# Kernel optimization log

Measured on AMD Instinct MI355X. Metric: run time of the kernel, lower is better.

Reference implementation:

```python
import jax, jax.numpy as jnp
import numpy as np

N = 1024
NEVAL = 131072
NUM_POLES = 8
DOMAIN = (-1.0, 1.0)
DOMAIN_LEN = DOMAIN[1] - DOMAIN[0]
EPS = 1e-14


def _cheb_nodes(n):
    # Chebyshev points of the second kind: cos(pi * linspace(0, 1, n))
    return jnp.cos(jnp.pi * jnp.linspace(0.0, 1.0, n))


def _to_standard(x):
    return 2.0 * (x - DOMAIN[0]) / DOMAIN_LEN - 1.0


def _barycentric_weights(nodes, poles_real, poles_imag):
    # Vectorized equivalent of the original per-node Python loop.
    n = nodes.shape[0]
    diff = nodes[:, None] - nodes[None, :]            # (N, N)
    eye = jnp.eye(n, dtype=bool)
    # log_weights[j] = -sum_{i!=j} log|nodes[j]-nodes[i]|
    log_w = -jnp.sum(jnp.log(jnp.where(eye, 1.0, jnp.abs(diff))), axis=1)
    # signs[j] = (-1)^(# of negative off-diagonal diffs); diagonal diff==0 contributes nothing
    neg_count = jnp.sum(diff < 0, axis=1)
    signs = jnp.where(neg_count % 2 == 0, 1.0, -1.0)
    # each conjugate pole pair contributes 2*log(sqrt((x-r)^2 + i^2)) = log((x-r)^2 + i^2)
    pole_term = jnp.log((nodes[:, None] - poles_real[None, :]) ** 2
                        + poles_imag[None, :] ** 2)   # (N, M)
    log_w = log_w + jnp.sum(pole_term, axis=1)
    log_w = log_w - jnp.max(log_w)
    w = signs * jnp.exp(log_w)
    return w / jnp.abs(w[0])


def setup_inputs() -> dict:
    key = jax.random.key(0)
    k1, k2, k3, k4 = jax.random.split(key, 4)
    x_eval = jax.random.uniform(k1, (NEVAL,), dtype=jnp.float32)  # in [0,1) subset of domain
    values = jax.random.normal(k2, (N,), dtype=jnp.float32)
    poles_real = jax.random.normal(k3, (NUM_POLES,), dtype=jnp.float32)
    poles_imag = jax.random.normal(k4, (NUM_POLES,), dtype=jnp.float32)
    return {"x_eval": x_eval, "values": values,
            "poles_real": poles_real, "poles_imag": poles_imag}


def reference(x_eval, values, poles_real, poles_imag):
    nodes = _cheb_nodes(N)
    nodes_std = _to_standard(nodes)                   # identity for domain (-1,1)
    w = _barycentric_weights(nodes, poles_real, poles_imag)

    x_std = _to_standard(x_eval)
    d_x = x_std[None, :] - nodes_std[:, None]         # (N, NEVAL)
    small = jnp.abs(d_x) < EPS
    small_any = jnp.any(small, axis=0)                # (NEVAL,)
    d_safe = jnp.where(small, 1.0, d_x)
    inv = jnp.where(small_any[None, :], 0.0, 1.0 / d_safe)
    inv = jnp.where(small, 1.0, inv)                  # exact-hit columns: indicator row -> 1

    num = jnp.einsum('n,nm,n->m', values, inv, w)
    den = jnp.einsum('nm,n->m', inv, w)
    return num / den
```

## Files before the change

### kernel.cpp

```cpp
#include <hip/hip_runtime.h>
#include <math.h>

#define N_NODES 1024
#define N_EVAL 131072
#define NUM_POLES 8
#define PI_D 3.14159265358979323846

__global__ void wk_setup(const float* __restrict__ values,
                         const float* __restrict__ poles_real,
                         const float* __restrict__ poles_imag,
                         float* __restrict__ nodes_f,
                         float* __restrict__ w_f,
                         float* __restrict__ wv_f) {
    const int j = threadIdx.x;
    const double nd = cos(PI_D * (double)j / (double)(N_NODES - 1));
    double prod = (j == 0 || j == N_NODES - 1) ? 0.5 : 1.0;
#pragma unroll
    for (int m = 0; m < NUM_POLES; ++m) {
        double dr = nd - (double)poles_real[m];
        double di = (double)poles_imag[m];
        prod *= dr * dr + di * di;
    }
    if (j & 1) prod = -prod;
    const float wf = (float)prod;
    nodes_f[j] = (float)nd;
    w_f[j] = wf;
    wv_f[j] = (float)(prod * (double)values[j]);
}

__global__ __launch_bounds__(256) void eval_kernel(
    const float* __restrict__ x_eval,
    const float* __restrict__ nodes_f,
    const float* __restrict__ w_f,
    const float* __restrict__ wv_f,
    float* __restrict__ out) {
    __shared__ __align__(16) float s_n[N_NODES];
    __shared__ __align__(16) float s_w[N_NODES];
    __shared__ __align__(16) float s_v[N_NODES];
    const int t = threadIdx.x;
    for (int k = t; k < N_NODES; k += 256) {
        s_n[k] = nodes_f[k];
        s_w[k] = w_f[k];
        s_v[k] = wv_f[k];
    }
    __syncthreads();

    const int i = blockIdx.x * 256 + t;
    const float x = x_eval[i];

    float num0 = 0.0f, den0 = 0.0f;
    float num1 = 0.0f, den1 = 0.0f;

    const float4* n4 = (const float4*)s_n;
    const float4* w4 = (const float4*)s_w;
    const float4* v4 = (const float4*)s_v;

#define BODY(C, NUM, DEN)                                                  \
    {                                                                      \
        float d = x - an.C;                                                \
        float r = __builtin_amdgcn_rcpf(d);                                \
        r = fmaf(r, fmaf(-d, r, 1.0f), r);              \
        NUM = fmaf(av.C, r, NUM);                                          \
        DEN = fmaf(aw.C, r, DEN);                                          \
    }

#pragma unroll 4
    for (int j4 = 0; j4 < N_NODES / 4; ++j4) {
        float4 an = n4[j4];
        float4 aw = w4[j4];
        float4 av = v4[j4];
        BODY(x, num0, den0)
        BODY(y, num1, den1)
        BODY(z, num0, den0)
        BODY(w, num1, den1)
    }
#undef BODY

    float res = (num0 + num1) / (den0 + den1);

    if (__builtin_expect(__builtin_isnan(res), 0)) {
        float hn = 0.0f, hd = 0.0f;
        for (int j = 0; j < N_NODES; ++j) {
            if (s_n[j] == x) { hn += s_v[j]; hd += s_w[j]; }
        }
        res = hn / hd;
    }
    out[i] = res;
}

extern "C" void kernel_launch(void* const* d_in, const int* in_sizes, int n_in,
                              void* d_out, int out_size, void* d_ws, size_t ws_size,
                              hipStream_t stream) {
    const float* x_eval     = (const float*)d_in[0];
    const float* values     = (const float*)d_in[1];
    const float* poles_real = (const float*)d_in[2];
    const float* poles_imag = (const float*)d_in[3];
    float* out = (float*)d_out;

    float* nodes_f = (float*)d_ws;
    float* w_f     = nodes_f + N_NODES;
    float* wv_f    = w_f + N_NODES;

    wk_setup<<<1, N_NODES, 0, stream>>>(values, poles_real, poles_imag,
                                        nodes_f, w_f, wv_f);
    eval_kernel<<<N_EVAL / 256, 256, 0, stream>>>(x_eval, nodes_f, w_f, wv_f, out);
}
```

Baseline: 145.3 us.

## Pair reciprocals into one rcp and split node sum across 4 lanes

New measurement: 130.3 us. 1.11x faster.

```diff
diff --git a/kernel.cpp b/kernel.cpp
--- a/kernel.cpp
+++ b/kernel.cpp
@@ -5,6 +5,10 @@
 #define N_EVAL 131072
 #define NUM_POLES 8
 #define PI_D 3.14159265358979323846
+
+#define CHUNKS 4
+#define CHUNK_N 256
+#define CHUNK_PAD 260
 
 __global__ void wk_setup(const float* __restrict__ values,
                          const float* __restrict__ poles_real,
@@ -22,70 +26,90 @@
         prod *= dr * dr + di * di;
     }
     if (j & 1) prod = -prod;
-    const float wf = (float)prod;
     nodes_f[j] = (float)nd;
-    w_f[j] = wf;
+    w_f[j] = (float)prod;
     wv_f[j] = (float)(prod * (double)values[j]);
 }
 
-__global__ __launch_bounds__(256) void eval_kernel(
+__global__ __launch_bounds__(256, 8) void eval_kernel(
     const float* __restrict__ x_eval,
     const float* __restrict__ nodes_f,
     const float* __restrict__ w_f,
     const float* __restrict__ wv_f,
     float* __restrict__ out) {
-    __shared__ __align__(16) float s_n[N_NODES];
-    __shared__ __align__(16) float s_w[N_NODES];
-    __shared__ __align__(16) float s_v[N_NODES];
+    __shared__ __align__(16) float s_n[CHUNKS * CHUNK_PAD];
+    __shared__ __align__(16) float s_w[CHUNKS * CHUNK_PAD];
+    __shared__ __align__(16) float s_v[CHUNKS * CHUNK_PAD];
     const int t = threadIdx.x;
-    for (int k = t; k < N_NODES; k += 256) {
-        s_n[k] = nodes_f[k];
-        s_w[k] = w_f[k];
-        s_v[k] = wv_f[k];
+#pragma unroll
+    for (int it = 0; it < 4; ++it) {
+        const int k = it * 256 + t;
+        const int idx = it * CHUNK_PAD + t;
+        s_n[idx] = nodes_f[k];
+        s_w[idx] = w_f[k];
+        s_v[idx] = wv_f[k];
     }
     __syncthreads();
 
-    const int i = blockIdx.x * 256 + t;
-    const float x = x_eval[i];
+    const int p = (blockIdx.x << 6) + (t >> 2);
+    const int c = t & 3;
+    const float x = x_eval[p];
+
+    const float4* n4 = (const float4*)(s_n + c * CHUNK_PAD);
+    const float4* w4 = (const float4*)(s_w + c * CHUNK_PAD);
+    const float4* v4 = (const float4*)(s_v + c * CHUNK_PAD);
 
     float num0 = 0.0f, den0 = 0.0f;
     float num1 = 0.0f, den1 = 0.0f;
 
-    const float4* n4 = (const float4*)s_n;
-    const float4* w4 = (const float4*)s_w;
-    const float4* v4 = (const float4*)s_v;
-
-#define BODY(C, NUM, DEN)                                                  \
-    {                                                                      \
-        float d = x - an.C;                                                \
-        float r = __builtin_amdgcn_rcpf(d);                                \
-        r = fmaf(r, fmaf(-d, r, 1.0f), r);              \
-        NUM = fmaf(av.C, r, NUM);                                          \
-        DEN = fmaf(aw.C, r, DEN);                                          \
+#pragma unroll 2
+    for (int q = 0; q < CHUNK_N / 4; ++q) {
+        const float4 an = n4[q];
+        const float4 aw = w4[q];
+        const float4 av = v4[q];
+        const float dx = x - an.x;
+        const float dy = x - an.y;
+        const float dz = x - an.z;
+        const float dw = x - an.w;
+        const float p0 = dx * dy;
+        const float p1 = dz * dw;
+        const float r0 = __builtin_amdgcn_rcpf(p0);
+        const float r1 = __builtin_amdgcn_rcpf(p1);
+        const float rx = r0 * dy;
+        const float ry = r0 * dx;
+        const float rz = r1 * dw;
+        const float rw = r1 * dz;
+        num0 = fmaf(av.x, rx, num0);
+        den0 = fmaf(aw.x, rx, den0);
+        num1 = fmaf(av.y, ry, num1);
+        den1 = fmaf(aw.y, ry, den1);
+        num0 = fmaf(av.z, rz, num0);
+        den0 = fmaf(aw.z, rz, den0);
+        num1 = fmaf(av.w, rw, num1);
+        den1 = fmaf(aw.w, rw, den1);
     }
 
-#pragma unroll 4
-    for (int j4 = 0; j4 < N_NODES / 4; ++j4) {
-        float4 an = n4[j4];
-        float4 aw = w4[j4];
-        float4 av = v4[j4];
-        BODY(x, num0, den0)
-        BODY(y, num1, den1)
-        BODY(z, num0, den0)
-        BODY(w, num1, den1)
+    float num = num0 + num1;
+    float den = den0 + den1;
+    num += __shfl_xor(num, 1);
+    den += __shfl_xor(den, 1);
+    num += __shfl_xor(num, 2);
+    den += __shfl_xor(den, 2);
+    float res = num / den;
+
+    if (c == 0) {
+        if (__builtin_expect(__builtin_isnan(res), 0)) {
+            float hn = 0.0f, hd = 0.0f;
+            for (int cc = 0; cc < CHUNKS; ++cc) {
+                for (int j = 0; j < CHUNK_N; ++j) {
+                    const int idx = cc * CHUNK_PAD + j;
+                    if (s_n[idx] == x) { hn += s_v[idx]; hd += s_w[idx]; }
+                }
+            }
+            res = hn / hd;
+        }
+        out[p] = res;
     }
-#undef BODY
-
-    float res = (num0 + num1) / (den0 + den1);
-
-    if (__builtin_expect(__builtin_isnan(res), 0)) {
-        float hn = 0.0f, hd = 0.0f;
-        for (int j = 0; j < N_NODES; ++j) {
-            if (s_n[j] == x) { hn += s_v[j]; hd += s_w[j]; }
-        }
-        res = hn / hd;
-    }
-    out[i] = res;
 }
 
 extern "C" void kernel_launch(void* const* d_in, const int* in_sizes, int n_in,
@@ -103,5 +127,5 @@
 
     wk_setup<<<1, N_NODES, 0, stream>>>(values, poles_real, poles_imag,
                                         nodes_f, w_f, wv_f);
-    eval_kernel<<<N_EVAL / 256, 256, 0, stream>>>(x_eval, nodes_f, w_f, wv_f, out);
+    eval_kernel<<<N_EVAL / 64, 256, 0, stream>>>(x_eval, nodes_f, w_f, wv_f, out);
 }
```

## Pair reciprocals, stream nodes via scalar loads, split node range across waves

Applied to the files above, without the earlier changes.

Measured after the change: 151.7 us. +4.4%, slower.

```diff
diff --git a/kernel.cpp b/kernel.cpp
--- a/kernel.cpp
+++ b/kernel.cpp
@@ -9,10 +9,8 @@
 __global__ void wk_setup(const float* __restrict__ values,
                          const float* __restrict__ poles_real,
                          const float* __restrict__ poles_imag,
-                         float* __restrict__ nodes_f,
-                         float* __restrict__ w_f,
-                         float* __restrict__ wv_f) {
-    const int j = threadIdx.x;
+                         float4* __restrict__ pk) {
+    const int j = blockIdx.x * 128 + threadIdx.x;
     const double nd = cos(PI_D * (double)j / (double)(N_NODES - 1));
     double prod = (j == 0 || j == N_NODES - 1) ? 0.5 : 1.0;
 #pragma unroll
@@ -22,70 +20,79 @@
         prod *= dr * dr + di * di;
     }
     if (j & 1) prod = -prod;
-    const float wf = (float)prod;
-    nodes_f[j] = (float)nd;
-    w_f[j] = wf;
-    wv_f[j] = (float)(prod * (double)values[j]);
+    pk[j] = make_float4((float)nd, (float)prod,
+                        (float)(prod * (double)values[j]), 0.0f);
 }
 
-__global__ __launch_bounds__(256) void eval_kernel(
+typedef float f16v __attribute__((ext_vector_type(16)));
+
+__global__ __launch_bounds__(256, 8) void eval_kernel(
     const float* __restrict__ x_eval,
-    const float* __restrict__ nodes_f,
-    const float* __restrict__ w_f,
-    const float* __restrict__ wv_f,
+    const float4* __restrict__ pk,
     float* __restrict__ out) {
-    __shared__ __align__(16) float s_n[N_NODES];
-    __shared__ __align__(16) float s_w[N_NODES];
-    __shared__ __align__(16) float s_v[N_NODES];
-    const int t = threadIdx.x;
-    for (int k = t; k < N_NODES; k += 256) {
-        s_n[k] = nodes_f[k];
-        s_w[k] = w_f[k];
-        s_v[k] = wv_f[k];
-    }
-    __syncthreads();
+    const int lane = threadIdx.x & 63;
+    const int wid  = threadIdx.x >> 6;
+    const int p = blockIdx.x * 64 + lane;
+    const float x = x_eval[p];
 
-    const int i = blockIdx.x * 256 + t;
-    const float x = x_eval[i];
+    unsigned long long up = (unsigned long long)(pk + wid * 256);
+    const unsigned lo = __builtin_amdgcn_readfirstlane((unsigned int)up);
+    const unsigned hi = __builtin_amdgcn_readfirstlane((unsigned int)(up >> 32));
+    const float4* tp = (const float4*)((((unsigned long long)hi) << 32) | lo);
 
     float num0 = 0.0f, den0 = 0.0f;
     float num1 = 0.0f, den1 = 0.0f;
 
-    const float4* n4 = (const float4*)s_n;
-    const float4* w4 = (const float4*)s_w;
-    const float4* v4 = (const float4*)s_v;
-
-#define BODY(C, NUM, DEN)                                                  \
+#define PAIR(nA, wA, vA, nB, wB, vB, NUM, DEN)                             \
     {                                                                      \
-        float d = x - an.C;                                                \
-        float r = __builtin_amdgcn_rcpf(d);                                \
-        r = fmaf(r, fmaf(-d, r, 1.0f), r);              \
-        NUM = fmaf(av.C, r, NUM);                                          \
-        DEN = fmaf(aw.C, r, DEN);                                          \
+        const float dA = x - (nA);                                         \
+        const float dB = x - (nB);                                         \
+        const float pp = dA * dB;                                          \
+        const float r = __builtin_amdgcn_rcpf(pp);                         \
+        const float rA = r * dB;                                           \
+        const float rB = r * dA;                                           \
+        NUM = fmaf((vA), rA, NUM);                                         \
+        DEN = fmaf((wA), rA, DEN);                                         \
+        NUM = fmaf((vB), rB, NUM);                                         \
+        DEN = fmaf((wB), rB, DEN);                                         \
     }
 
-#pragma unroll 4
-    for (int j4 = 0; j4 < N_NODES / 4; ++j4) {
-        float4 an = n4[j4];
-        float4 aw = w4[j4];
-        float4 av = v4[j4];
-        BODY(x, num0, den0)
-        BODY(y, num1, den1)
-        BODY(z, num0, den0)
-        BODY(w, num1, den1)
+    for (int it = 0; it < 32; ++it) {
+        f16v ta, tb;
+        asm volatile(
+            "s_load_dwordx16 %0, %2, 0x0\n\t"
+            "s_load_dwordx16 %1, %2, 0x40\n\t"
+            "s_waitcnt lgkmcnt(0)"
+            : "=&s"(ta), "=&s"(tb)
+            : "s"(tp));
+        PAIR(ta[0], ta[1], ta[2], ta[4], ta[5], ta[6], num0, den0)
+        PAIR(ta[8], ta[9], ta[10], ta[12], ta[13], ta[14], num1, den1)
+        PAIR(tb[0], tb[1], tb[2], tb[4], tb[5], tb[6], num0, den0)
+        PAIR(tb[8], tb[9], tb[10], tb[12], tb[13], tb[14], num1, den1)
+        tp += 8;
     }
-#undef BODY
+#undef PAIR
 
-    float res = (num0 + num1) / (den0 + den1);
+    __shared__ float rn[4][64];
+    __shared__ float rd[4][64];
+    rn[wid][lane] = num0 + num1;
+    rd[wid][lane] = den0 + den1;
+    __syncthreads();
 
-    if (__builtin_expect(__builtin_isnan(res), 0)) {
-        float hn = 0.0f, hd = 0.0f;
-        for (int j = 0; j < N_NODES; ++j) {
-            if (s_n[j] == x) { hn += s_v[j]; hd += s_w[j]; }
+    if (wid == 0) {
+        const float nn = (rn[0][lane] + rn[1][lane]) + (rn[2][lane] + rn[3][lane]);
+        const float dd = (rd[0][lane] + rd[1][lane]) + (rd[2][lane] + rd[3][lane]);
+        float res = nn / dd;
+        if (__builtin_expect(__builtin_isnan(res), 0)) {
+            float hn = 0.0f, hd = 0.0f;
+            for (int j = 0; j < N_NODES; ++j) {
+                const float4 e = pk[j];
+                if (e.x == x) { hn += e.z; hd += e.y; }
+            }
+            res = hn / hd;
         }
-        res = hn / hd;
+        out[p] = res;
     }
-    out[i] = res;
 }
 
 extern "C" void kernel_launch(void* const* d_in, const int* in_sizes, int n_in,
@@ -97,11 +104,8 @@
     const float* poles_imag = (const float*)d_in[3];
     float* out = (float*)d_out;
 
-    float* nodes_f = (float*)d_ws;
-    float* w_f     = nodes_f + N_NODES;
-    float* wv_f    = w_f + N_NODES;
+    float4* pk = (float4*)d_ws;
 
-    wk_setup<<<1, N_NODES, 0, stream>>>(values, poles_real, poles_imag,
-                                        nodes_f, w_f, wv_f);
-    eval_kernel<<<N_EVAL / 256, 256, 0, stream>>>(x_eval, nodes_f, w_f, wv_f, out);
+    wk_setup<<<8, 128, 0, stream>>>(values, poles_real, poles_imag, pk);
+    eval_kernel<<<N_EVAL / 64, 256, 0, stream>>>(x_eval, pk, out);
 }
```

## Fuse weight setup into eval kernel and split nodes across waves with register blocking

Applied to the files above, without the earlier changes.

Measured after the change: 125.9 us. 1.15x faster.

```diff
diff --git a/kernel.cpp b/kernel.cpp
--- a/kernel.cpp
+++ b/kernel.cpp
@@ -6,86 +6,102 @@
 #define NUM_POLES 8
 #define PI_D 3.14159265358979323846
 
-__global__ void wk_setup(const float* __restrict__ values,
-                         const float* __restrict__ poles_real,
-                         const float* __restrict__ poles_imag,
-                         float* __restrict__ nodes_f,
-                         float* __restrict__ w_f,
-                         float* __restrict__ wv_f) {
-    const int j = threadIdx.x;
-    const double nd = cos(PI_D * (double)j / (double)(N_NODES - 1));
-    double prod = (j == 0 || j == N_NODES - 1) ? 0.5 : 1.0;
-#pragma unroll
-    for (int m = 0; m < NUM_POLES; ++m) {
-        double dr = nd - (double)poles_real[m];
-        double di = (double)poles_imag[m];
-        prod *= dr * dr + di * di;
-    }
-    if (j & 1) prod = -prod;
-    const float wf = (float)prod;
-    nodes_f[j] = (float)nd;
-    w_f[j] = wf;
-    wv_f[j] = (float)(prod * (double)values[j]);
-}
-
-__global__ __launch_bounds__(256) void eval_kernel(
+__global__ __launch_bounds__(512, 4) void eval_kernel(
     const float* __restrict__ x_eval,
-    const float* __restrict__ nodes_f,
-    const float* __restrict__ w_f,
-    const float* __restrict__ wv_f,
+    const float* __restrict__ values,
+    const float* __restrict__ poles_real,
+    const float* __restrict__ poles_imag,
     float* __restrict__ out) {
     __shared__ __align__(16) float s_n[N_NODES];
     __shared__ __align__(16) float s_w[N_NODES];
     __shared__ __align__(16) float s_v[N_NODES];
+    __shared__ float2 s_r[8][256];
+
     const int t = threadIdx.x;
-    for (int k = t; k < N_NODES; k += 256) {
-        s_n[k] = nodes_f[k];
-        s_w[k] = w_f[k];
-        s_v[k] = wv_f[k];
+
+#pragma unroll
+    for (int h = 0; h < 2; ++h) {
+        const int j = t + h * 512;
+        const double nd = cos(PI_D * (double)j / (double)(N_NODES - 1));
+        double prod = (j == 0 || j == N_NODES - 1) ? 0.5 : 1.0;
+#pragma unroll
+        for (int m = 0; m < NUM_POLES; ++m) {
+            const double dr = nd - (double)poles_real[m];
+            const double di = (double)poles_imag[m];
+            prod *= dr * dr + di * di;
+        }
+        if (j & 1) prod = -prod;
+        s_n[j] = (float)nd;
+        s_w[j] = (float)prod;
+        s_v[j] = (float)(prod * (double)values[j]);
     }
     __syncthreads();
 
-    const int i = blockIdx.x * 256 + t;
-    const float x = x_eval[i];
+    const int lane = t & 63;
+    const int wid  = t >> 6;
+    const int pbase = blockIdx.x * 256;
+    const float x0 = x_eval[pbase + lane];
+    const float x1 = x_eval[pbase + 64 + lane];
+    const float x2 = x_eval[pbase + 128 + lane];
+    const float x3 = x_eval[pbase + 192 + lane];
 
-    float num0 = 0.0f, den0 = 0.0f;
-    float num1 = 0.0f, den1 = 0.0f;
+    const float4* n4 = (const float4*)s_n + wid * 32;
+    const float4* w4 = (const float4*)s_w + wid * 32;
+    const float4* v4 = (const float4*)s_v + wid * 32;
 
-    const float4* n4 = (const float4*)s_n;
-    const float4* w4 = (const float4*)s_w;
-    const float4* v4 = (const float4*)s_v;
+    float a0 = 0.0f, b0 = 0.0f, a1 = 0.0f, b1 = 0.0f;
+    float a2 = 0.0f, b2 = 0.0f, a3 = 0.0f, b3 = 0.0f;
 
-#define BODY(C, NUM, DEN)                                                  \
+#define NODE(C)                                                            \
     {                                                                      \
-        float d = x - an.C;                                                \
-        float r = __builtin_amdgcn_rcpf(d);                                \
-        r = fmaf(r, fmaf(-d, r, 1.0f), r);              \
-        NUM = fmaf(av.C, r, NUM);                                          \
-        DEN = fmaf(aw.C, r, DEN);                                          \
+        const float d0 = x0 - an.C;                                        \
+        const float d1 = x1 - an.C;                                        \
+        const float d2 = x2 - an.C;                                        \
+        const float d3 = x3 - an.C;                                        \
+        const float r0 = __builtin_amdgcn_rcpf(d0);                        \
+        const float r1 = __builtin_amdgcn_rcpf(d1);                        \
+        const float r2 = __builtin_amdgcn_rcpf(d2);                        \
+        const float r3 = __builtin_amdgcn_rcpf(d3);                        \
+        a0 = fmaf(av.C, r0, a0); b0 = fmaf(aw.C, r0, b0);                  \
+        a1 = fmaf(av.C, r1, a1); b1 = fmaf(aw.C, r1, b1);                  \
+        a2 = fmaf(av.C, r2, a2); b2 = fmaf(aw.C, r2, b2);                  \
+        a3 = fmaf(av.C, r3, a3); b3 = fmaf(aw.C, r3, b3);                  \
     }
 
 #pragma unroll 4
-    for (int j4 = 0; j4 < N_NODES / 4; ++j4) {
-        float4 an = n4[j4];
-        float4 aw = w4[j4];
-        float4 av = v4[j4];
-        BODY(x, num0, den0)
-        BODY(y, num1, den1)
-        BODY(z, num0, den0)
-        BODY(w, num1, den1)
+    for (int q = 0; q < 32; ++q) {
+        const float4 an = n4[q];
+        const float4 aw = w4[q];
+        const float4 av = v4[q];
+        NODE(x) NODE(y) NODE(z) NODE(w)
     }
-#undef BODY
+#undef NODE
 
-    float res = (num0 + num1) / (den0 + den1);
+    s_r[wid][lane]       = make_float2(a0, b0);
+    s_r[wid][lane + 64]  = make_float2(a1, b1);
+    s_r[wid][lane + 128] = make_float2(a2, b2);
+    s_r[wid][lane + 192] = make_float2(a3, b3);
+    __syncthreads();
 
-    if (__builtin_expect(__builtin_isnan(res), 0)) {
-        float hn = 0.0f, hd = 0.0f;
-        for (int j = 0; j < N_NODES; ++j) {
-            if (s_n[j] == x) { hn += s_v[j]; hd += s_w[j]; }
+    if (t < 256) {
+        float nn = 0.0f, dd = 0.0f;
+#pragma unroll
+        for (int w = 0; w < 8; ++w) {
+            const float2 pr = s_r[w][t];
+            nn += pr.x;
+            dd += pr.y;
         }
-        res = hn / hd;
+        float res = nn / dd;
+        if (__builtin_expect(__builtin_isnan(res), 0)) {
+            const float x = x_eval[pbase + t];
+            float hn = 0.0f, hd = 0.0f;
+            for (int j = 0; j < N_NODES; ++j) {
+                if (s_n[j] == x) { hn += s_v[j]; hd += s_w[j]; }
+            }
+            res = hn / hd;
+        }
+        out[pbase + t] = res;
     }
-    out[i] = res;
 }
 
 extern "C" void kernel_launch(void* const* d_in, const int* in_sizes, int n_in,
@@ -97,11 +113,6 @@
     const float* poles_imag = (const float*)d_in[3];
     float* out = (float*)d_out;
 
-    float* nodes_f = (float*)d_ws;
-    float* w_f     = nodes_f + N_NODES;
-    float* wv_f    = w_f + N_NODES;
-
-    wk_setup<<<1, N_NODES, 0, stream>>>(values, poles_real, poles_imag,
-                                        nodes_f, w_f, wv_f);
-    eval_kernel<<<N_EVAL / 256, 256, 0, stream>>>(x_eval, nodes_f, w_f, wv_f, out);
+    eval_kernel<<<N_EVAL / 256, 512, 0, stream>>>(x_eval, values,
+                                                  poles_real, poles_imag, out);
 }
```
